# Kernel optimization log

Measured on AMD Instinct MI355X. Metric: run time of the kernel, lower is better.

The kernel has to match this reference:

```python
import jax, jax.numpy as jnp
import numpy as np

N = 50000
E = 800000
IN_C = 128
HID = 128
OUT_C = 128
EPS = 1e-5


def _glorot(key, shape):
    fan_in = shape[-1]
    return jax.random.normal(key, shape, dtype=jnp.float32) / jnp.sqrt(jnp.float32(fan_in))


def setup_inputs() -> dict:
    key = jax.random.key(0)
    ks = jax.random.split(key, 16)
    inp = {
        'x': jax.random.normal(ks[0], (N, IN_C), dtype=jnp.float32),
        'edge_index': jax.random.randint(ks[1], (2, E), 0, N, dtype=jnp.int64),
    }
    dims = [(IN_C, HID), (HID, HID), (HID, OUT_C)]
    for i, (din, dout) in enumerate(dims, start=1):
        inp[f'Wl{i}'] = _glorot(ks[2 * i], (dout, din))      # applied to aggregated neighbors
        inp[f'bl{i}'] = jnp.zeros((dout,), dtype=jnp.float32)
        inp[f'Wr{i}'] = _glorot(ks[2 * i + 1], (dout, din))  # applied to root node
        inp[f'g{i}'] = jnp.ones((dout,), dtype=jnp.float32)   # BN gamma
        inp[f'b{i}'] = jnp.zeros((dout,), dtype=jnp.float32)  # BN beta
    inp['Wlin'] = _glorot(ks[10], (OUT_C, 2 * HID + OUT_C))
    inp['blin'] = jnp.zeros((OUT_C,), dtype=jnp.float32)
    return inp


def _sage(x, src, dst, Wl, bl, Wr):
    # mean aggregation of source features at target nodes (PyG SAGEConv default)
    msg = x[src]                                              # [E, C]
    s = jax.ops.segment_sum(msg, dst, num_segments=N)         # [N, C]
    cnt = jax.ops.segment_sum(jnp.ones((src.shape[0], 1), x.dtype), dst, num_segments=N)
    aggr = s / jnp.maximum(cnt, 1.0)
    return aggr @ Wl.T + bl + x @ Wr.T


def _bn(x, g, b):
    # training-mode BatchNorm1d over the node dimension
    mu = jnp.mean(x, axis=0)
    var = jnp.var(x, axis=0)
    return g * (x - mu) * jax.lax.rsqrt(var + EPS) + b


def reference(x, edge_index, Wl1, bl1, Wr1, g1, b1, Wl2, bl2, Wr2, g2, b2,
              Wl3, bl3, Wr3, g3, b3, Wlin, blin):
    src, dst = edge_index[0], edge_index[1]
    x1 = _bn(jax.nn.relu(_sage(x, src, dst, Wl1, bl1, Wr1)), g1, b1)
    x2 = _bn(jax.nn.relu(_sage(x1, src, dst, Wl2, bl2, Wr2)), g2, b2)
    x3 = _bn(jax.nn.relu(_sage(x2, src, dst, Wl3, bl3, Wr3)), g3, b3)
    cat = jnp.concatenate([x1, x2, x3], axis=-1)              # [N, 2*HID + OUT_C]
    return jax.nn.relu(cat @ Wlin.T + blin)
```

## Files before the change

kernel.cpp:

```cpp
#include <hip/hip_runtime.h>

#define NN 50000
#define NE 800000
#define CH 128
#define EPSV 1e-5f
#define NPASS 2
#define PRANGE 25000

typedef unsigned short ushort_t;
typedef __attribute__((ext_vector_type(8))) short short8_t;
typedef __attribute__((ext_vector_type(8))) unsigned short u16x8;
typedef __attribute__((ext_vector_type(4))) float f32x4;

__device__ inline float bf2f(ushort_t u) {
    union { unsigned int i; float f; } t; t.i = ((unsigned int)u) << 16; return t.f;
}
__device__ inline ushort_t f2bf(float f) {
    union { float f; unsigned int i; } t; t.f = f;
    unsigned int r = t.i + 0x7fff + ((t.i >> 16) & 1);
    return (ushort_t)(r >> 16);
}


__global__ void k_hist(const int* __restrict__ dst, int* __restrict__ deg) {
    int e = blockIdx.x * 256 + threadIdx.x;
    if (e < NE) atomicAdd(&deg[dst[e]], 1);
}

__global__ void k_scan(int* __restrict__ deg, int* __restrict__ row_ptr) {
    __shared__ int wsum[16];
    const int t = threadIdx.x;
    const int lane = t & 63;
    const int wid = t >> 6;
    int carry = 0;
    for (int base = 0; base < NN; base += 1024) {
        int i = base + t;
        int v = (i < NN) ? deg[i] : 0;
        if (i < NN) deg[i] = 0;
        int x = v;
        #pragma unroll
        for (int off = 1; off < 64; off <<= 1) {
            int y = __shfl_up(x, off, 64);
            if (lane >= off) x += y;
        }
        if (lane == 63) wsum[wid] = x;
        __syncthreads();
        if (wid == 0 && lane < 16) {
            int s = wsum[lane];
            #pragma unroll
            for (int off = 1; off < 16; off <<= 1) {
                int y = __shfl_up(s, off, 16);
                if (lane >= off) s += y;
            }
            wsum[lane] = s;
        }
        __syncthreads();
        int wbase = (wid > 0) ? wsum[wid - 1] : 0;
        if (i < NN) row_ptr[i] = carry + wbase + x - v;
        carry += wsum[15];
        __syncthreads();
    }
    if (t == 0) row_ptr[NN] = carry;
}

__global__ void k_fillp(const int* __restrict__ src, const int* __restrict__ dst,
                        const int* __restrict__ row_ptr, int* __restrict__ fillc,
                        int* __restrict__ csr, int lo, int hi) {
    int e = blockIdx.x * 256 + threadIdx.x;
    if (e < NE) {
        int d = dst[e];
        int s = src[e];
        if (d >= lo && d < hi) {
            int pos = row_ptr[d] + atomicAdd(&fillc[d], 1);
            csr[pos] = s;
        }
    }
}


__global__ __launch_bounds__(256) void k_cvtX(const float* __restrict__ x,
                                              ushort_t* __restrict__ xb,
                                              float* __restrict__ bn_sums) {
    int i = blockIdx.x * 256 + threadIdx.x;
    if (blockIdx.x == 0) {
        bn_sums[threadIdx.x] = 0.f;
        bn_sums[256 + threadIdx.x] = 0.f;
        bn_sums[512 + threadIdx.x] = 0.f;
    }
    if (i >= NN * 32) return;
    float4 v = ((const float4*)x)[i];
    ushort4 o;
    o.x = f2bf(v.x); o.y = f2bf(v.y); o.z = f2bf(v.z); o.w = f2bf(v.w);
    ((ushort4*)xb)[i] = o;
}

__global__ __launch_bounds__(256) void k_pack2(const float* __restrict__ s0,
                                               const float* __restrict__ s1,
                                               ushort_t* __restrict__ dst) {
    int t = blockIdx.x * 256 + threadIdx.x;
    if (t >= 128 * 256) return;
    int o = t >> 8, k = t & 255;
    float v = (k < 128) ? s0[o * 128 + k] : s1[o * 128 + k - 128];
    dst[t] = f2bf(v);
}

__global__ void k_foldnext(const float* __restrict__ bn_sums,
                           const float* __restrict__ g, const float* __restrict__ b,
                           const float* __restrict__ Wl, const float* __restrict__ Wr,
                           const float* __restrict__ bl,
                           ushort_t* __restrict__ Wp, float* __restrict__ bias,
                           float* __restrict__ abg) {
    __shared__ float red[128];
    int o = blockIdx.x;
    int k = threadIdx.x;
    float mu = bn_sums[k] * (1.0f / NN);
    float var = bn_sums[128 + k] * (1.0f / NN) - mu * mu;
    var = var > 0.f ? var : 0.f;
    float a = g[k] * rsqrtf(var + EPSV);
    float c = b[k] - a * mu;
    if (o == 0) { abg[k] = a; abg[128 + k] = c; }
    float wr = Wr[o * 128 + k];
    Wp[o * 256 + k]       = f2bf(Wl[o * 128 + k]);
    Wp[o * 256 + 128 + k] = f2bf(wr * a);
    red[k] = wr * c;
    __syncthreads();
    for (int s = 64; s > 0; s >>= 1) {
        if (k < s) red[k] += red[k + s];
        __syncthreads();
    }
    if (k == 0) bias[o] = bl[o] + red[0];
}

__global__ void k_foldF(const float* __restrict__ bn3,
                        const float* __restrict__ g3, const float* __restrict__ b3,
                        const float* __restrict__ ab1, const float* __restrict__ ab2,
                        const float* __restrict__ Wlin, const float* __restrict__ blin,
                        ushort_t* __restrict__ Wp, float* __restrict__ bias) {
    __shared__ float red[128];
    int o = blockIdx.x;
    int k = threadIdx.x;
    float mu = bn3[k] * (1.0f / NN);
    float var = bn3[128 + k] * (1.0f / NN) - mu * mu;
    var = var > 0.f ? var : 0.f;
    float a3 = g3[k] * rsqrtf(var + EPSV);
    float c3 = b3[k] - a3 * mu;
    float w1 = Wlin[o * 384 + k];
    float w2 = Wlin[o * 384 + 128 + k];
    float w3 = Wlin[o * 384 + 256 + k];
    Wp[o * 384 + k]       = f2bf(w1 * ab1[k]);
    Wp[o * 384 + 128 + k] = f2bf(w2 * ab2[k]);
    Wp[o * 384 + 256 + k] = f2bf(w3 * a3);
    red[k] = w1 * ab1[128 + k] + w2 * ab2[128 + k] + w3 * c3;
    __syncthreads();
    for (int s = 64; s > 0; s >>= 1) {
        if (k < s) red[k] += red[k + s];
        __syncthreads();
    }
    if (k == 0) bias[o] = blin[o] + red[0];
}


template<bool FOLD>
__global__ __launch_bounds__(256) void k_aggr(const ushort_t* __restrict__ x,
        const int* __restrict__ row_ptr, const int* __restrict__ csr,
        const float* __restrict__ ab, ushort_t* __restrict__ aggr) {
    const int node = blockIdx.x * 4 + (threadIdx.x >> 6);
    const int lane = threadIdx.x & 63;
    const int l4 = lane & 15;
    const int q  = lane >> 4;
    const int r0 = row_ptr[node], r1 = row_ptr[node + 1];
    const int d = r1 - r0;
    const ushort_t* xrow = x + l4 * 8;

    float accA[8] = {0, 0, 0, 0, 0, 0, 0, 0};
    float accB[8] = {0, 0, 0, 0, 0, 0, 0, 0};

    int j = r0 + q;
    for (; j + 12 < r1; j += 16) {
        int s0 = csr[j], s1 = csr[j + 4], s2 = csr[j + 8], s3 = csr[j + 12];
        u16x8 v0 = *(const u16x8*)(xrow + (size_t)s0 * CH);
        u16x8 v1 = *(const u16x8*)(xrow + (size_t)s1 * CH);
        u16x8 v2 = *(const u16x8*)(xrow + (size_t)s2 * CH);
        u16x8 v3 = *(const u16x8*)(xrow + (size_t)s3 * CH);
        #pragma unroll
        for (int i = 0; i < 8; ++i) {
            accA[i] += bf2f(v0[i]) + bf2f(v1[i]);
            accB[i] += bf2f(v2[i]) + bf2f(v3[i]);
        }
    }
    for (; j < r1; j += 4) {
        int s0 = csr[j];
        u16x8 v0 = *(const u16x8*)(xrow + (size_t)s0 * CH);
        #pragma unroll
        for (int i = 0; i < 8; ++i) accA[i] += bf2f(v0[i]);
    }

    const float sc = d > 0 ? 1.0f / (float)d : 0.0f;
    #pragma unroll
    for (int i = 0; i < 8; ++i) {
        float s = accA[i] + accB[i];
        s += __shfl_xor(s, 16);
        s += __shfl_xor(s, 32);
        accA[i] = s * sc;
    }

    if (q == 0) {
        u16x8 ov;
        #pragma unroll
        for (int i = 0; i < 8; ++i) {
            float v = accA[i];
            if (FOLD) v = d > 0 ? fmaf(v, ab[l4 * 8 + i], ab[128 + l4 * 8 + i]) : 0.f;
            ov[i] = f2bf(v);
        }
        *(u16x8*)&aggr[(size_t)node * CH + l4 * 8] = ov;
    }
}


#define STAGE(buf, t) do {                                                           \
    const ushort_t* Ab_ = (((t) >> 1) == 0) ? A0 : ((((t) >> 1) == 1) ? A1 : A2);    \
    Ab_ += ((t) & 1) * 64;                                                           \
    const ushort_t* Wb_ = W + (t) * 64;                                              \
    _Pragma("unroll")                                                                \
    for (int i_ = 0; i_ < 4; ++i_) {                                                 \
        int f_ = i_ * 256 + tid;                                                     \
        int row_ = f_ >> 3;                                                          \
        int c_ = (f_ & 7) ^ (row_ & 7);                                              \
        int gr_ = bn0 + row_; gr_ = gr_ < NN ? gr_ : NN - 1;                         \
        __builtin_amdgcn_global_load_lds(                                            \
            (const __attribute__((address_space(1))) unsigned int*)(Ab_ + (size_t)gr_ * CH + c_ * 8), \
            (__attribute__((address_space(3))) unsigned int*)(&Abuf[buf][f_ * 8]),   \
            16, 0, 0);                                                               \
        __builtin_amdgcn_global_load_lds(                                            \
            (const __attribute__((address_space(1))) unsigned int*)(Wb_ + (size_t)row_ * (NT * 64) + c_ * 8), \
            (__attribute__((address_space(3))) unsigned int*)(&Wbuf[buf][f_ * 8]),   \
            16, 0, 0);                                                               \
    } } while (0)

template<int NT, bool STATS, bool F32OUT>
__global__ __launch_bounds__(256, 2) void k_mgemm(
    const ushort_t* __restrict__ A0, const ushort_t* __restrict__ A1,
    const ushort_t* __restrict__ A2,
    const ushort_t* __restrict__ W, const float* __restrict__ bias,
    ushort_t* __restrict__ outb, float* __restrict__ outf,
    float* __restrict__ bn_sums)
{
    __shared__ __align__(16) ushort_t Abuf[2][128 * 64];
    __shared__ __align__(16) ushort_t Wbuf[2][128 * 64];
    __shared__ float bns[128], bnq[128];

    const int tid  = threadIdx.x;
    const int lane = tid & 63;
    const int wid  = tid >> 6;
    const int l15  = lane & 15;
    const int lg   = lane >> 4;
    const int wn   = (wid >> 1) * 64;
    const int wo   = (wid & 1) * 64;
    const int bn0  = blockIdx.x * 128;

    if (STATS && tid < 128) { bns[tid] = 0.f; bnq[tid] = 0.f; }

    f32x4 acc[4][4];
    #pragma unroll
    for (int i = 0; i < 4; ++i)
        #pragma unroll
        for (int j = 0; j < 4; ++j)
            acc[i][j] = (f32x4){0.f, 0.f, 0.f, 0.f};

    STAGE(0, 0);
    asm volatile("s_waitcnt vmcnt(0)");
    __syncthreads();

    #pragma unroll
    for (int t = 0; t < NT; ++t) {
        const int cur = t & 1;
        if (t + 1 < NT) STAGE(cur ^ 1, t + 1);
        #pragma unroll
        for (int s = 0; s < 2; ++s) {
            short8_t af[4], wf[4];
            #pragma unroll
            for (int b = 0; b < 4; ++b) {
                int ra = wn + b * 16 + l15;
                int ca = (s * 4 + lg) ^ (ra & 7);
                af[b] = *(const short8_t*)&Abuf[cur][ra * 64 + ca * 8];
                int rw = wo + b * 16 + l15;
                int cw = (s * 4 + lg) ^ (rw & 7);
                wf[b] = *(const short8_t*)&Wbuf[cur][rw * 64 + cw * 8];
            }
            #pragma unroll
            for (int i = 0; i < 4; ++i)
                #pragma unroll
                for (int j = 0; j < 4; ++j)
                    acc[i][j] = __builtin_amdgcn_mfma_f32_16x16x32_bf16(
                        af[i], wf[j], acc[i][j], 0, 0, 0);
        }
        asm volatile("s_waitcnt vmcnt(0)");
        __syncthreads();
    }

    float bv[4];
    #pragma unroll
    for (int j = 0; j < 4; ++j) bv[j] = bias[wo + j * 16 + l15];

    float sum[4] = {0.f, 0.f, 0.f, 0.f}, sq[4] = {0.f, 0.f, 0.f, 0.f};

    #pragma unroll
    for (int i = 0; i < 4; ++i) {
        #pragma unroll
        for (int r = 0; r < 4; ++r) {
            int gn = bn0 + wn + i * 16 + lg * 4 + r;
            bool ok = gn < NN;
            #pragma unroll
            for (int j = 0; j < 4; ++j) {
                int o = wo + j * 16 + l15;
                float v = acc[i][j][r] + bv[j];
                v = fmaxf(v, 0.f);
                if (ok) {
                    if (F32OUT) outf[(size_t)gn * CH + o] = v;
                    else        outb[(size_t)gn * CH + o] = f2bf(v);
                    if (STATS) { sum[j] += v; sq[j] += v * v; }
                }
            }
        }
    }

    if (STATS) {
        #pragma unroll
        for (int j = 0; j < 4; ++j) {
            float ss = sum[j], qq = sq[j];
            ss += __shfl_xor(ss, 16); qq += __shfl_xor(qq, 16);
            ss += __shfl_xor(ss, 32); qq += __shfl_xor(qq, 32);
            if (lg == 0) {
                atomicAdd(&bns[wo + j * 16 + l15], ss);
                atomicAdd(&bnq[wo + j * 16 + l15], qq);
            }
        }
        __syncthreads();
        if (tid < 128) {
            atomicAdd(&bn_sums[tid], bns[tid]);
            atomicAdd(&bn_sums[128 + tid], bnq[tid]);
        }
    }
}


extern "C" void kernel_launch(void* const* d_in, const int* in_sizes, int n_in,
                              void* d_out, int out_size, void* d_ws, size_t ws_size,
                              hipStream_t stream) {
    const float* x  = (const float*)d_in[0];
    const int*   ei = (const int*)d_in[1];
    const int* esrc = ei;
    const int* edst = ei + NE;

    const float* Wl[3] = {(const float*)d_in[2],  (const float*)d_in[7],  (const float*)d_in[12]};
    const float* bl[3] = {(const float*)d_in[3],  (const float*)d_in[8],  (const float*)d_in[13]};
    const float* Wr[3] = {(const float*)d_in[4],  (const float*)d_in[9],  (const float*)d_in[14]};
    const float* gg[3] = {(const float*)d_in[5],  (const float*)d_in[10], (const float*)d_in[15]};
    const float* bb[3] = {(const float*)d_in[6],  (const float*)d_in[11], (const float*)d_in[16]};
    const float* Wlin  = (const float*)d_in[17];
    const float* blin  = (const float*)d_in[18];

    float* fo = (float*)d_out;

    const size_t NC = (size_t)NN * CH;
    ushort_t* xb     = (ushort_t*)d_ws;
    ushort_t* y1b    = xb + NC;
    ushort_t* y2b    = y1b + NC;
    ushort_t* y3b    = y2b + NC;
    ushort_t* aggr_b = y3b + NC;
    ushort_t* Wp1    = aggr_b + NC;
    ushort_t* Wp2    = Wp1 + 128 * 256;
    ushort_t* Wp3    = Wp2 + 128 * 256;
    ushort_t* WpF    = Wp3 + 128 * 256;
    float* bias2     = (float*)(WpF + 128 * 384);
    float* bias3     = bias2 + 128;
    float* biasF     = bias3 + 128;
    float* bn_sums   = biasF + 128;
    float* ab        = bn_sums + 768;
    int* row_ptr     = (int*)(ab + 512);
    int* fillc       = row_ptr + NN + 1;
    int* csr         = fillc + NN;

    hipMemsetAsync(fillc, 0, NN * sizeof(int), stream);
    k_hist<<<(NE + 255) / 256, 256, 0, stream>>>(edst, fillc);
    k_scan<<<1, 1024, 0, stream>>>(fillc, row_ptr);
    for (int p = 0; p < NPASS; ++p)
        k_fillp<<<NE / 256, 256, 0, stream>>>(esrc, edst, row_ptr, fillc, csr,
                                              p * PRANGE, (p + 1) * PRANGE);

    k_cvtX<<<(NN * 32 + 255) / 256, 256, 0, stream>>>(x, xb, bn_sums);
    k_pack2<<<128, 256, 0, stream>>>(Wl[0], Wr[0], Wp1);

    const int GEMM_GRID = (NN + 127) / 128;

    k_aggr<false><<<NN / 4, 256, 0, stream>>>(xb, row_ptr, csr, nullptr, aggr_b);
    k_mgemm<4, true, false><<<GEMM_GRID, 256, 0, stream>>>(
        aggr_b, xb, nullptr, Wp1, bl[0], y1b, nullptr, bn_sums);
    k_foldnext<<<128, 128, 0, stream>>>(bn_sums, gg[0], bb[0],
                                        Wl[1], Wr[1], bl[1], Wp2, bias2, ab);

    k_aggr<true><<<NN / 4, 256, 0, stream>>>(y1b, row_ptr, csr, ab, aggr_b);
    k_mgemm<4, true, false><<<GEMM_GRID, 256, 0, stream>>>(
        aggr_b, y1b, nullptr, Wp2, bias2, y2b, nullptr, bn_sums + 256);
    k_foldnext<<<128, 128, 0, stream>>>(bn_sums + 256, gg[1], bb[1],
                                        Wl[2], Wr[2], bl[2], Wp3, bias3, ab + 256);

    k_aggr<true><<<NN / 4, 256, 0, stream>>>(y2b, row_ptr, csr, ab + 256, aggr_b);
    k_mgemm<4, true, false><<<GEMM_GRID, 256, 0, stream>>>(
        aggr_b, y2b, nullptr, Wp3, bias3, y3b, nullptr, bn_sums + 512);
    k_foldF<<<128, 128, 0, stream>>>(bn_sums + 512, gg[2], bb[2], ab, ab + 256,
                                     Wlin, blin, WpF, biasF);

    k_mgemm<6, false, true><<<GEMM_GRID, 256, 0, stream>>>(
        y1b, y2b, y3b, WpF, biasF, nullptr, fo, nullptr);
}
```

Baseline: 362.7 us.

## Bucket CSR edges by source range and give each node a quarter-wave in aggregation

The CSR is rebuilt so each destination's neighbour list is split into 7 buckets by source-index range (src>>13), using a per-(node,bucket) histogram, scan and fill. The aim is for all nodes in a wave to gather from roughly the same source region at the same time, improving L2 locality. The aggregation kernel now gives one 16-lane group per node (16 nodes per block) instead of one wave per node, which removes the cross-lane shuffle reduction. The x-to-bf16 conversion and the first weight pack are merged into one launch. In exchange, the counter and row-pointer arrays grow sevenfold, the scan does more work, and each lane group now walks one node's edges serially with less memory-level parallelism per node.

```diff
diff --git a/kernel.cpp b/kernel.cpp
--- a/kernel.cpp
+++ b/kernel.cpp
@@ -4,6 +4,8 @@
 #define NE 800000
 #define CH 128
 #define EPSV 1e-5f
+#define NPH 7
+#define PSHIFT 13
 #define NPASS 2
 #define PRANGE 25000
 
@@ -22,12 +24,13 @@
 }
 
 
-__global__ void k_hist(const int* __restrict__ dst, int* __restrict__ deg) {
+__global__ void k_hist2(const int* __restrict__ src, const int* __restrict__ dst,
+                        int* __restrict__ deg2) {
     int e = blockIdx.x * 256 + threadIdx.x;
-    if (e < NE) atomicAdd(&deg[dst[e]], 1);
-}
-
-__global__ void k_scan(int* __restrict__ deg, int* __restrict__ row_ptr) {
+    if (e < NE) atomicAdd(&deg2[dst[e] * NPH + (src[e] >> PSHIFT)], 1);
+}
+
+__global__ void k_scan2(int* __restrict__ deg2, int* __restrict__ rp2) {
     __shared__ int wsum[16];
     const int t = threadIdx.x;
     const int lane = t & 63;
@@ -35,8 +38,16 @@
     int carry = 0;
     for (int base = 0; base < NN; base += 1024) {
         int i = base + t;
-        int v = (i < NN) ? deg[i] : 0;
-        if (i < NN) deg[i] = 0;
+        int d[NPH];
+        int v = 0;
+        if (i < NN) {
+            #pragma unroll
+            for (int c = 0; c < NPH; ++c) {
+                d[c] = deg2[i * NPH + c];
+                v += d[c];
+                deg2[i * NPH + c] = 0;
+            }
+        }
         int x = v;
         #pragma unroll
         for (int off = 1; off < 64; off <<= 1) {
@@ -56,52 +67,58 @@
         }
         __syncthreads();
         int wbase = (wid > 0) ? wsum[wid - 1] : 0;
-        if (i < NN) row_ptr[i] = carry + wbase + x - v;
+        if (i < NN) {
+            int run = carry + wbase + x - v;
+            #pragma unroll
+            for (int c = 0; c < NPH; ++c) {
+                rp2[i * NPH + c] = run;
+                run += d[c];
+            }
+        }
         carry += wsum[15];
         __syncthreads();
     }
-    if (t == 0) row_ptr[NN] = carry;
+    if (t == 0) rp2[NN * NPH] = carry;
 }
 
 __global__ void k_fillp(const int* __restrict__ src, const int* __restrict__ dst,
-                        const int* __restrict__ row_ptr, int* __restrict__ fillc,
+                        const int* __restrict__ rp2, int* __restrict__ fillc2,
                         int* __restrict__ csr, int lo, int hi) {
     int e = blockIdx.x * 256 + threadIdx.x;
     if (e < NE) {
         int d = dst[e];
         int s = src[e];
         if (d >= lo && d < hi) {
-            int pos = row_ptr[d] + atomicAdd(&fillc[d], 1);
+            int slot = d * NPH + (s >> PSHIFT);
+            int pos = rp2[slot] + atomicAdd(&fillc2[slot], 1);
             csr[pos] = s;
         }
     }
 }
 
 
-__global__ __launch_bounds__(256) void k_cvtX(const float* __restrict__ x,
-                                              ushort_t* __restrict__ xb,
-                                              float* __restrict__ bn_sums) {
-    int i = blockIdx.x * 256 + threadIdx.x;
-    if (blockIdx.x == 0) {
-        bn_sums[threadIdx.x] = 0.f;
-        bn_sums[256 + threadIdx.x] = 0.f;
-        bn_sums[512 + threadIdx.x] = 0.f;
-    }
-    if (i >= NN * 32) return;
-    float4 v = ((const float4*)x)[i];
-    ushort4 o;
-    o.x = f2bf(v.x); o.y = f2bf(v.y); o.z = f2bf(v.z); o.w = f2bf(v.w);
-    ((ushort4*)xb)[i] = o;
-}
-
-__global__ __launch_bounds__(256) void k_pack2(const float* __restrict__ s0,
-                                               const float* __restrict__ s1,
-                                               ushort_t* __restrict__ dst) {
-    int t = blockIdx.x * 256 + threadIdx.x;
-    if (t >= 128 * 256) return;
-    int o = t >> 8, k = t & 255;
-    float v = (k < 128) ? s0[o * 128 + k] : s1[o * 128 + k - 128];
-    dst[t] = f2bf(v);
+__global__ __launch_bounds__(256) void k_cvtpack(const float* __restrict__ x,
+        ushort_t* __restrict__ xb, const float* __restrict__ s0,
+        const float* __restrict__ s1, ushort_t* __restrict__ Wp1,
+        float* __restrict__ bn_sums) {
+    if (blockIdx.x < 6250) {
+        int i = blockIdx.x * 256 + threadIdx.x;
+        if (blockIdx.x == 0) {
+            bn_sums[threadIdx.x] = 0.f;
+            bn_sums[256 + threadIdx.x] = 0.f;
+            bn_sums[512 + threadIdx.x] = 0.f;
+        }
+        if (i >= NN * 32) return;
+        float4 v = ((const float4*)x)[i];
+        ushort4 o;
+        o.x = f2bf(v.x); o.y = f2bf(v.y); o.z = f2bf(v.z); o.w = f2bf(v.w);
+        ((ushort4*)xb)[i] = o;
+    } else {
+        int t = (blockIdx.x - 6250) * 256 + threadIdx.x;
+        int o = t >> 8, k = t & 255;
+        float v = (k < 128) ? s0[o * 128 + k] : s1[o * 128 + k - 128];
+        Wp1[t] = f2bf(v);
+    }
 }
 
 __global__ void k_foldnext(const float* __restrict__ bn_sums,
@@ -162,58 +179,48 @@
 
 template<bool FOLD>
 __global__ __launch_bounds__(256) void k_aggr(const ushort_t* __restrict__ x,
-        const int* __restrict__ row_ptr, const int* __restrict__ csr,
+        const int* __restrict__ rp2, const int* __restrict__ csr,
         const float* __restrict__ ab, ushort_t* __restrict__ aggr) {
-    const int node = blockIdx.x * 4 + (threadIdx.x >> 6);
     const int lane = threadIdx.x & 63;
-    const int l4 = lane & 15;
-    const int q  = lane >> 4;
-    const int r0 = row_ptr[node], r1 = row_ptr[node + 1];
-    const int d = r1 - r0;
+    const int q    = lane >> 4;
+    const int l4   = lane & 15;
+    const int node = blockIdx.x * 16 + (threadIdx.x >> 6) * 4 + q;
     const ushort_t* xrow = x + l4 * 8;
 
-    float accA[8] = {0, 0, 0, 0, 0, 0, 0, 0};
-    float accB[8] = {0, 0, 0, 0, 0, 0, 0, 0};
-
-    int j = r0 + q;
-    for (; j + 12 < r1; j += 16) {
-        int s0 = csr[j], s1 = csr[j + 4], s2 = csr[j + 8], s3 = csr[j + 12];
-        u16x8 v0 = *(const u16x8*)(xrow + (size_t)s0 * CH);
-        u16x8 v1 = *(const u16x8*)(xrow + (size_t)s1 * CH);
-        u16x8 v2 = *(const u16x8*)(xrow + (size_t)s2 * CH);
-        u16x8 v3 = *(const u16x8*)(xrow + (size_t)s3 * CH);
-        #pragma unroll
-        for (int i = 0; i < 8; ++i) {
-            accA[i] += bf2f(v0[i]) + bf2f(v1[i]);
-            accB[i] += bf2f(v2[i]) + bf2f(v3[i]);
-        }
-    }
-    for (; j < r1; j += 4) {
-        int s0 = csr[j];
-        u16x8 v0 = *(const u16x8*)(xrow + (size_t)s0 * CH);
-        #pragma unroll
-        for (int i = 0; i < 8; ++i) accA[i] += bf2f(v0[i]);
-    }
-
-    const float sc = d > 0 ? 1.0f / (float)d : 0.0f;
+    float acc[8] = {0, 0, 0, 0, 0, 0, 0, 0};
+
+    int a = rp2[node * NPH];
+    const int r0 = a;
+    for (int p = 1; p <= NPH; ++p) {
+        const int b = rp2[node * NPH + p];
+        int j = a;
+        for (; j + 1 < b; j += 2) {
+            int s0 = csr[j], s1 = csr[j + 1];
+            u16x8 v0 = *(const u16x8*)(xrow + (size_t)s0 * CH);
+            u16x8 v1 = *(const u16x8*)(xrow + (size_t)s1 * CH);
+            #pragma unroll
+            for (int i = 0; i < 8; ++i)
+                acc[i] += bf2f(v0[i]) + bf2f(v1[i]);
+        }
+        if (j < b) {
+            int s0 = csr[j];
+            u16x8 v0 = *(const u16x8*)(xrow + (size_t)s0 * CH);
+            #pragma unroll
+            for (int i = 0; i < 8; ++i) acc[i] += bf2f(v0[i]);
+        }
+        a = b;
+    }
+
+    const int deg = a - r0;
+    const float sc = deg > 0 ? 1.0f / (float)deg : 0.0f;
+    u16x8 ov;
     #pragma unroll
     for (int i = 0; i < 8; ++i) {
-        float s = accA[i] + accB[i];
-        s += __shfl_xor(s, 16);
-        s += __shfl_xor(s, 32);
-        accA[i] = s * sc;
-    }
-
-    if (q == 0) {
-        u16x8 ov;
-        #pragma unroll
-        for (int i = 0; i < 8; ++i) {
-            float v = accA[i];
-            if (FOLD) v = d > 0 ? fmaf(v, ab[l4 * 8 + i], ab[128 + l4 * 8 + i]) : 0.f;
-            ov[i] = f2bf(v);
-        }
-        *(u16x8*)&aggr[(size_t)node * CH + l4 * 8] = ov;
-    }
+        float v = acc[i] * sc;
+        if (FOLD) v = deg > 0 ? fmaf(v, ab[l4 * 8 + i], ab[128 + l4 * 8 + i]) : 0.f;
+        ov[i] = f2bf(v);
+    }
+    *(u16x8*)&aggr[(size_t)node * CH + l4 * 8] = ov;
 }
 
 
@@ -377,35 +384,35 @@
     float* biasF     = bias3 + 128;
     float* bn_sums   = biasF + 128;
     float* ab        = bn_sums + 768;
-    int* row_ptr     = (int*)(ab + 512);
-    int* fillc       = row_ptr + NN + 1;
-    int* csr         = fillc + NN;
-
-    hipMemsetAsync(fillc, 0, NN * sizeof(int), stream);
-    k_hist<<<(NE + 255) / 256, 256, 0, stream>>>(edst, fillc);
-    k_scan<<<1, 1024, 0, stream>>>(fillc, row_ptr);
+    int* deg2        = (int*)(ab + 512);
+    int* rp2         = deg2 + NN * NPH;
+    int* csr         = rp2 + NN * NPH + 1;
+
+    hipMemsetAsync(deg2, 0, NN * NPH * sizeof(int), stream);
+    k_hist2<<<(NE + 255) / 256, 256, 0, stream>>>(esrc, edst, deg2);
+    k_scan2<<<1, 1024, 0, stream>>>(deg2, rp2);
     for (int p = 0; p < NPASS; ++p)
-        k_fillp<<<NE / 256, 256, 0, stream>>>(esrc, edst, row_ptr, fillc, csr,
+        k_fillp<<<NE / 256, 256, 0, stream>>>(esrc, edst, rp2, deg2, csr,
                                               p * PRANGE, (p + 1) * PRANGE);
 
-    k_cvtX<<<(NN * 32 + 255) / 256, 256, 0, stream>>>(x, xb, bn_sums);
-    k_pack2<<<128, 256, 0, stream>>>(Wl[0], Wr[0], Wp1);
+    k_cvtpack<<<6250 + 128, 256, 0, stream>>>(x, xb, Wl[0], Wr[0], Wp1, bn_sums);
 
     const int GEMM_GRID = (NN + 127) / 128;
-
-    k_aggr<false><<<NN / 4, 256, 0, stream>>>(xb, row_ptr, csr, nullptr, aggr_b);
+    const int AGGR_GRID = NN / 16;
+
+    k_aggr<false><<<AGGR_GRID, 256, 0, stream>>>(xb, rp2, csr, nullptr, aggr_b);
     k_mgemm<4, true, false><<<GEMM_GRID, 256, 0, stream>>>(
         aggr_b, xb, nullptr, Wp1, bl[0], y1b, nullptr, bn_sums);
     k_foldnext<<<128, 128, 0, stream>>>(bn_sums, gg[0], bb[0],
                                         Wl[1], Wr[1], bl[1], Wp2, bias2, ab);
 
-    k_aggr<true><<<NN / 4, 256, 0, stream>>>(y1b, row_ptr, csr, ab, aggr_b);
+    k_aggr<true><<<AGGR_GRID, 256, 0, stream>>>(y1b, rp2, csr, ab, aggr_b);
     k_mgemm<4, true, false><<<GEMM_GRID, 256, 0, stream>>>(
         aggr_b, y1b, nullptr, Wp2, bias2, y2b, nullptr, bn_sums + 256);
     k_foldnext<<<128, 128, 0, stream>>>(bn_sums + 256, gg[1], bb[1],
                                         Wl[2], Wr[2], bl[2], Wp3, bias3, ab + 256);
 
-    k_aggr<true><<<NN / 4, 256, 0, stream>>>(y2b, row_ptr, csr, ab + 256, aggr_b);
+    k_aggr<true><<<AGGR_GRID, 256, 0, stream>>>(y2b, rp2, csr, ab + 256, aggr_b);
     k_mgemm<4, true, false><<<GEMM_GRID, 256, 0, stream>>>(
         aggr_b, y2b, nullptr, Wp3, bias3, y3b, nullptr, bn_sums + 512);
     k_foldF<<<128, 128, 0, stream>>>(bn_sums + 512, gg[2], bb[2], ab, ab + 256,
```

Result: slower. 407.8 us (+12.4%).
